# Performance work log

Hardware: AMD Instinct MI355X
Metric: run time of the kernel (lower is better)

Reference implementation:

```python
import jax, jax.numpy as jnp
import numpy as np
from math import lgamma

# ---- constants matching init_kwargs ----
HID_DIM = 512
LAT_DIM = 128
KAPPA = 50.0
NORM_EPS = 1.0
NORM_MAX = 2.0
BATCH = 65536

# ---- host-side constant KLD (scipy-free log Bessel via series) ----
def _log_iv(nu, k, M=300):
    m = np.arange(M)
    lg_fact = np.array([lgamma(i + 1.0) for i in m])
    lg_gam = np.array([lgamma(i + nu + 1.0) for i in m])
    logt = (2.0 * m + nu) * np.log(k / 2.0) - lg_fact - lg_gam
    mx = logt.max()
    return mx + np.log(np.exp(logt - mx).sum())

def _vmf_kld(k, d):
    # k*((iv(d/2+1,k)+iv(d/2,k)*d/(2k))/iv(d/2,k) - d/(2k)) + d*log(k)/2 - log(iv(d/2,k)) - loggamma(d/2+1) - d*log(2)/2
    ratio = np.exp(_log_iv(d / 2.0 + 1.0, k) - _log_iv(d / 2.0, k))
    return (k * (ratio + d / (2.0 * k) - d / (2.0 * k))
            + d * np.log(k) / 2.0 - _log_iv(d / 2.0, k)
            - lgamma(d / 2.0 + 1.0) - d * np.log(2.0) / 2.0)

def _uniform_kld(x1, x2, y1, y2):
    return np.log((y2 - y1) / (x2 - x1))

KLD_CONST = float(_vmf_kld(KAPPA, LAT_DIM) + _uniform_kld(0.0, NORM_EPS, 0.0, NORM_MAX))

# ---- batched vMF rejection sampling for the scalar weight w ----
def _sample_weight_batch(key, kappa, dim, shape):
    d = float(dim - 1)
    b = d / (np.sqrt(4.0 * kappa ** 2 + d * d) + 2.0 * kappa)
    x = (1.0 - b) / (1.0 + b)
    c = kappa * x + d * np.log(1.0 - x * x)

    def cond(st):
        return jnp.logical_not(jnp.all(st[2]))

    def body(st):
        key, w, acc = st
        key, kz, ku = jax.random.split(key, 3)
        z = jax.random.beta(kz, d / 2.0, d / 2.0, shape)
        wn = (1.0 - (1.0 + b) * z) / (1.0 - (1.0 - b) * z)
        u = jax.random.uniform(ku, shape)
        ok = (kappa * wn + d * jnp.log(1.0 - x * wn) - c) >= jnp.log(u)
        w = jnp.where(jnp.logical_and(jnp.logical_not(acc), ok), wn, w)
        return (key, w, jnp.logical_or(acc, ok))

    st0 = (key, jnp.zeros(shape, jnp.float32), jnp.zeros(shape, bool))
    _, w, _ = jax.lax.while_loop(cond, body, st0)
    return w


def setup_inputs() -> dict:
    key = jax.random.key(0)
    k1, k2 = jax.random.split(key)
    lat_code = jax.random.normal(k1, (BATCH, HID_DIM), dtype=jnp.float32)
    W_mu = jax.random.normal(k2, (LAT_DIM, HID_DIM), dtype=jnp.float32) * 0.02
    b_mu = jnp.zeros((LAT_DIM,), dtype=jnp.float32)
    return {"lat_code": lat_code, "W_mu": W_mu, "b_mu": b_mu, "n_sample": 4}


def reference(lat_code, W_mu, b_mu, n_sample):
    B = lat_code.shape[0]
    # estimate_param (norm_func=False branch)
    mu_lin = lat_code @ W_mu.T + b_mu                       # (B, L)
    norm = jnp.linalg.norm(mu_lin, axis=1, keepdims=True)   # (B, 1)
    redundant_norm = (1.0 - norm) ** 2                      # (B, 1)
    mu = mu_lin / norm                                      # unit directions

    # sample_cell, vectorized over (n_sample, B)
    kw, kv, kn = jax.random.split(jax.random.key(1), 3)
    w = _sample_weight_batch(kw, KAPPA, LAT_DIM, (n_sample, B))[..., None]  # (n,B,1)
    v = jax.random.normal(kv, (n_sample, B, LAT_DIM), dtype=jnp.float32)
    dot = jnp.sum(mu * v, axis=-1, keepdims=True)                           # (n,B,1)
    mu_n = jnp.linalg.norm(mu, axis=-1, keepdims=True)                      # ~1
    ortho = v - mu * (dot / mu_n)
    v_orth = ortho / jnp.linalg.norm(ortho, axis=-1, keepdims=True)
    noise = jax.random.uniform(kn, (n_sample, B, 1)) * NORM_EPS             # add_norm_noise
    norm_with_noise = 1.0 + noise                                           # norm=ones branch
    vecs = (v_orth * jnp.sqrt(1.0 - w * w) + mu * w) * norm_with_noise      # (n,B,L)

    kld = jnp.full((B,), KLD_CONST, dtype=lat_code.dtype)
    return (vecs, kld, mu, redundant_norm)
```

## Files before the change

kernel.cpp:

```cpp
#include <hip/hip_runtime.h>
#include <cmath>
#include <cstdint>


#define BTOT 65536
#define NSAMP 4
#define HID 512
#define LATD 128
#define NW 262144u

typedef _Float16 half8 __attribute__((ext_vector_type(8)));
typedef _Float16 half4 __attribute__((ext_vector_type(4)));
typedef float f32x4 __attribute__((ext_vector_type(4)));

__host__ __device__ __forceinline__ uint32_t rotl32(uint32_t v, int r){
  return (v << r) | (v >> (32 - r));
}

__host__ __device__ __forceinline__ void tf2(uint32_t k0, uint32_t k1,
                                             uint32_t x0, uint32_t x1,
                                             uint32_t& o0, uint32_t& o1){
  uint32_t ks2 = k0 ^ k1 ^ 0x1BD11BDAu;
  x0 += k0; x1 += k1;
  x0+=x1; x1=rotl32(x1,13); x1^=x0;
  x0+=x1; x1=rotl32(x1,15); x1^=x0;
  x0+=x1; x1=rotl32(x1,26); x1^=x0;
  x0+=x1; x1=rotl32(x1, 6); x1^=x0;
  x0+=k1; x1+=ks2+1u;
  x0+=x1; x1=rotl32(x1,17); x1^=x0;
  x0+=x1; x1=rotl32(x1,29); x1^=x0;
  x0+=x1; x1=rotl32(x1,16); x1^=x0;
  x0+=x1; x1=rotl32(x1,24); x1^=x0;
  x0+=ks2; x1+=k0+2u;
  x0+=x1; x1=rotl32(x1,13); x1^=x0;
  x0+=x1; x1=rotl32(x1,15); x1^=x0;
  x0+=x1; x1=rotl32(x1,26); x1^=x0;
  x0+=x1; x1=rotl32(x1, 6); x1^=x0;
  x0+=k0; x1+=k1+3u;
  x0+=x1; x1=rotl32(x1,17); x1^=x0;
  x0+=x1; x1=rotl32(x1,29); x1^=x0;
  x0+=x1; x1=rotl32(x1,16); x1^=x0;
  x0+=x1; x1=rotl32(x1,24); x1^=x0;
  x0+=k1; x1+=ks2+4u;
  x0+=x1; x1=rotl32(x1,13); x1^=x0;
  x0+=x1; x1=rotl32(x1,15); x1^=x0;
  x0+=x1; x1=rotl32(x1,26); x1^=x0;
  x0+=x1; x1=rotl32(x1, 6); x1^=x0;
  x0+=ks2; x1+=k0+5u;
  o0 = x0; o1 = x1;
}

__device__ __forceinline__ uint2 mkk(uint32_t a, uint32_t b){ uint2 r; r.x=a; r.y=b; return r; }

__device__ __forceinline__ uint2 p_split(uint2 k, uint32_t i){
  uint32_t o0,o1; tf2(k.x,k.y,0u,i,o0,o1); return mkk(o0,o1);
}
__device__ __forceinline__ uint32_t p_bits(uint2 k, uint32_t i){
  uint32_t o0,o1; tf2(k.x,k.y,0u,i,o0,o1); return o0^o1;
}

__device__ __forceinline__ float u01(uint32_t bits){
  return __uint_as_float((bits >> 9) | 0x3f800000u) - 1.0f;
}

__device__ __forceinline__ float erfinv_f(float x){
  float w = -log1pf(-x*x);
  float p;
  if (w < 5.0f){
    w -= 2.5f;
    p = 2.81022636e-08f;
    p = fmaf(p,w, 3.43273939e-07f);
    p = fmaf(p,w,-3.5233877e-06f);
    p = fmaf(p,w,-4.39150654e-06f);
    p = fmaf(p,w, 0.00021858087f);
    p = fmaf(p,w,-0.00125372503f);
    p = fmaf(p,w,-0.00417768164f);
    p = fmaf(p,w, 0.246640727f);
    p = fmaf(p,w, 1.50140941f);
  } else {
    w = sqrtf(w) - 3.0f;
    p = -0.000200214257f;
    p = fmaf(p,w, 0.000100950558f);
    p = fmaf(p,w, 0.00134934322f);
    p = fmaf(p,w,-0.00367342844f);
    p = fmaf(p,w, 0.00573950773f);
    p = fmaf(p,w,-0.0076224613f);
    p = fmaf(p,w, 0.00943887047f);
    p = fmaf(p,w, 1.00167406f);
    p = fmaf(p,w, 2.83297682f);
  }
  return p * x;
}

__device__ __forceinline__ float jnorm_from_bits(uint32_t bits){
  const float lo = -0.99999994f;
  float f = u01(bits);
  float un = fmaxf(lo, f*2.0f + lo);
  return 1.41421356f * erfinv_f(un);
}

__device__ __forceinline__ float jnorm_fast(uint32_t bits){
  const float lo = -0.99999994f;
  float f = u01(bits);
  float x = fmaxf(lo, f*2.0f + lo);
  float w = -0.69314718f * __builtin_amdgcn_logf(fmaf(-x, x, 1.0f));
  float p;
  if (w < 5.0f){
    w -= 2.5f;
    p = 2.81022636e-08f;
    p = fmaf(p,w, 3.43273939e-07f);
    p = fmaf(p,w,-3.5233877e-06f);
    p = fmaf(p,w,-4.39150654e-06f);
    p = fmaf(p,w, 0.00021858087f);
    p = fmaf(p,w,-0.00125372503f);
    p = fmaf(p,w,-0.00417768164f);
    p = fmaf(p,w, 0.246640727f);
    p = fmaf(p,w, 1.50140941f);
  } else {
    w = __builtin_amdgcn_sqrtf(w) - 3.0f;
    p = -0.000200214257f;
    p = fmaf(p,w, 0.000100950558f);
    p = fmaf(p,w, 0.00134934322f);
    p = fmaf(p,w,-0.00367342844f);
    p = fmaf(p,w, 0.00573950773f);
    p = fmaf(p,w,-0.0076224613f);
    p = fmaf(p,w, 0.00943887047f);
    p = fmaf(p,w, 1.00167406f);
    p = fmaf(p,w, 2.83297682f);
  }
  return 1.41421356f * (p * x);
}

__device__ float loggamma_a635(uint2 ek){
  const float dg = 63.5f - (1.0f/3.0f);
  const float cg = (1.0f/3.0f) / sqrtf(dg);
  uint2 key = p_split(ek, 0);
  float lg = 0.0f;
  for (int it=0; it<64; ++it){
    uint2 xk = p_split(key, 1);
    uint2 uk = p_split(key, 2);
    uint2 sub2 = p_split(xk, 1);
    float x = 1.41421356f * erfinv_f(fmaxf(-0.99999994f,
                u01(p_bits(sub2, 0))*2.0f + (-0.99999994f)));
    float v = 1.0f + x*cg;
    float X = x*x;
    float V = v*v*v;
    float U = u01(p_bits(uk, 0));
    bool rej = (U >= 1.0f - 0.0331f*(X*X)) &&
               (logf(U) >= 0.5f*X + dg*((1.0f - V) + logf(V)));
    if (!rej){ lg = logf(dg) + logf(V); break; }
    key = p_split(key, 0);
  }
  return lg;
}

__global__ __launch_bounds__(256) void bprep_kernel(const float* __restrict__ W,
                                                    unsigned short* __restrict__ Bhi,
                                                    unsigned short* __restrict__ Blo){
  int t = blockIdx.x*256 + threadIdx.x;
  int l = t >> 7, k4 = t & 127;
  int k0 = k4*4;
  float4 wv = *(const float4*)(W + (size_t)l*HID + k0);
  half4 h, lo;
  float b0 = (float)(_Float16)wv.x; h.x = (_Float16)wv.x; lo.x = (_Float16)((wv.x-b0)*2048.0f);
  float b1 = (float)(_Float16)wv.y; h.y = (_Float16)wv.y; lo.y = (_Float16)((wv.y-b1)*2048.0f);
  float b2 = (float)(_Float16)wv.z; h.z = (_Float16)wv.z; lo.z = (_Float16)((wv.z-b2)*2048.0f);
  float b3 = (float)(_Float16)wv.w; h.w = (_Float16)wv.w; lo.w = (_Float16)((wv.w-b3)*2048.0f);
  int c = k0 >> 5, g = (k0 & 31) >> 3, j0 = k0 & 7;
  int nf = l >> 4, n15 = l & 15;
  size_t idx = ((size_t)((c*8 + nf)*4 + g)*16 + n15)*8 + j0;
  *(half4*)(Bhi + idx) = h;
  *(half4*)(Blo + idx) = lo;
}

__global__ __launch_bounds__(256) void mu_kernel(const float* __restrict__ lat,
                                                 const unsigned short* __restrict__ Bhi_g,
                                                 const unsigned short* __restrict__ Blo_g,
                                                 const float* __restrict__ bmu,
                                                 float* __restrict__ muo,
                                                 float* __restrict__ kldo,
                                                 float* __restrict__ rno,
                                                 float kldv){
  __shared__ __align__(16) char smem[26624];
  _Float16* Ahi = (_Float16*)smem;
  _Float16* Alo = (_Float16*)(smem + 5120);
  _Float16* Blh = (_Float16*)(smem + 10240);
  _Float16* Bll = (_Float16*)(smem + 18432);

  const int tid = threadIdx.x;
  const int w   = tid >> 6;
  const int lane = tid & 63;
  const int q = lane >> 4, n15 = lane & 15;
  const int b0 = blockIdx.x * 64;
  const float4* latg = (const float4*)lat;

  f32x4 acc1a[4][2], acc1b[4][2], acc2[4][2];
  #pragma unroll
  for (int rf=0;rf<4;++rf)
    #pragma unroll
    for (int nl=0;nl<2;++nl){
      acc1a[rf][nl] = (f32x4)0.0f;
      acc1b[rf][nl] = (f32x4)0.0f;
      acc2[rf][nl]  = (f32x4)0.0f;
    }

  for (int c=0;c<16;++c){
    __syncthreads();
    #pragma unroll
    for (int p=0;p<2;++p){
      int flat = p*256 + tid;
      int row = flat >> 3, k4 = flat & 7;
      float4 lv = latg[(size_t)(b0+row)*(HID/4) + c*8 + k4];
      half4 h, lo;
      float r0=(float)(_Float16)lv.x; h.x=(_Float16)lv.x; lo.x=(_Float16)((lv.x-r0)*2048.0f);
      float r1=(float)(_Float16)lv.y; h.y=(_Float16)lv.y; lo.y=(_Float16)((lv.y-r1)*2048.0f);
      float r2=(float)(_Float16)lv.z; h.z=(_Float16)lv.z; lo.z=(_Float16)((lv.z-r2)*2048.0f);
      float r3=(float)(_Float16)lv.w; h.w=(_Float16)lv.w; lo.w=(_Float16)((lv.w-r3)*2048.0f);
      *(half4*)(Ahi + row*40 + k4*4) = h;
      *(half4*)(Alo + row*40 + k4*4) = lo;
    }
    {
      const short4* sh = (const short4*)Bhi_g + (size_t)c*1024;
      const short4* sl = (const short4*)Blo_g + (size_t)c*1024;
      short4* dh = (short4*)Blh;
      short4* dl = (short4*)Bll;
      #pragma unroll
      for (int p=0;p<4;++p){
        dh[tid + p*256] = sh[tid + p*256];
        dl[tid + p*256] = sl[tid + p*256];
      }
    }
    __syncthreads();

    half8 bh[2], bl[2];
    #pragma unroll
    for (int nl=0;nl<2;++nl){
      int nf = w*2 + nl;
      bh[nl] = *(const half8*)(Blh + ((nf*4 + q)*16 + n15)*8);
      bl[nl] = *(const half8*)(Bll + ((nf*4 + q)*16 + n15)*8);
    }
    #pragma unroll
    for (int rf=0;rf<4;++rf){
      half8 ah = *(const half8*)(Ahi + (rf*16 + n15)*40 + q*8);
      half8 al = *(const half8*)(Alo + (rf*16 + n15)*40 + q*8);
      #pragma unroll
      for (int nl=0;nl<2;++nl){
        if (c < 8)
          acc1a[rf][nl] = __builtin_amdgcn_mfma_f32_16x16x32_f16(ah, bh[nl], acc1a[rf][nl], 0,0,0);
        else
          acc1b[rf][nl] = __builtin_amdgcn_mfma_f32_16x16x32_f16(ah, bh[nl], acc1b[rf][nl], 0,0,0);
        acc2[rf][nl] = __builtin_amdgcn_mfma_f32_16x16x32_f16(ah, bl[nl], acc2[rf][nl], 0,0,0);
        acc2[rf][nl] = __builtin_amdgcn_mfma_f32_16x16x32_f16(al, bh[nl], acc2[rf][nl], 0,0,0);
      }
    }
  }

  __syncthreads();
  double* nbuf  = (double*)smem;
  double* normd = (double*)(smem + 2048);

  double bias[2];
  #pragma unroll
  for (int nl=0;nl<2;++nl) bias[nl] = (double)bmu[w*32 + nl*16 + n15];

  double val[4][2][4];
  double part[4][4];
  #pragma unroll
  for (int rf=0;rf<4;++rf){
    #pragma unroll
    for (int r=0;r<4;++r){
      double s = 0.0;
      #pragma unroll
      for (int nl=0;nl<2;++nl){
        double v = (double)acc1a[rf][nl][r] + (double)acc1b[rf][nl][r]
                 + (double)acc2[rf][nl][r]*(1.0/2048.0) + bias[nl];
        val[rf][nl][r] = v;
        s += v*v;
      }
      part[rf][r] = s;
    }
  }
  #pragma unroll
  for (int rf=0;rf<4;++rf)
    #pragma unroll
    for (int r=0;r<4;++r){
      double t = part[rf][r];
      t += __shfl_xor(t, 1, 64);
      t += __shfl_xor(t, 2, 64);
      t += __shfl_xor(t, 4, 64);
      t += __shfl_xor(t, 8, 64);
      part[rf][r] = t;
    }
  if (n15 == 0){
    #pragma unroll
    for (int rf=0;rf<4;++rf)
      #pragma unroll
      for (int r=0;r<4;++r)
        nbuf[w*64 + rf*16 + q*4 + r] = part[rf][r];
  }
  __syncthreads();
  if (tid < 64){
    double tot = nbuf[tid] + nbuf[64+tid] + nbuf[128+tid] + nbuf[192+tid];
    double nd = sqrt(tot);
    normd[tid] = nd;
    double om = 1.0 - nd;
    rno[b0 + tid]  = (float)(om*om);
    kldo[b0 + tid] = kldv;
  }
  __syncthreads();
  #pragma unroll
  for (int rf=0;rf<4;++rf){
    #pragma unroll
    for (int r=0;r<4;++r){
      double nd = normd[rf*16 + q*4 + r];
      int m = b0 + rf*16 + q*4 + r;
      #pragma unroll
      for (int nl=0;nl<2;++nl)
        muo[(size_t)m*LATD + w*32 + nl*16 + n15] = (float)(val[rf][nl][r]/nd);
    }
  }
}

__global__ __launch_bounds__(256) void wood_kernel(float* __restrict__ wbuf,
                                                   float* __restrict__ nwnbuf,
                                                   uint2 kw, uint2 kn,
                                                   float onepb, float onemb,
                                                   float xf, float cf){
  uint32_t j = blockIdx.x*256u + threadIdx.x;
  nwnbuf[j] = 1.0f + u01(p_bits(kn, j));
  uint2 key = kw;
  float w = 0.0f;
  for (int it=0; it<64; ++it){
    uint2 kz = p_split(key, 1);
    uint2 ku = p_split(key, 2);
    uint2 ka = p_split(kz, 0);
    uint2 kb = p_split(kz, 1);
    float lga = loggamma_a635(p_split(ka, j));
    float lgb = loggamma_a635(p_split(kb, j));
    float mx  = fmaxf(lga, lgb);
    float lab = mx + log1pf(expf(-fabsf(lga-lgb)));
    float z   = expf(lga - lab);
    float wn  = (1.0f - onepb*z) / (1.0f - onemb*z);
    float u   = u01(p_bits(ku, j));
    bool ok = (50.0f*wn + 127.0f*logf(1.0f - xf*wn) - cf) >= logf(u);
    if (ok){ w = wn; break; }
    key = p_split(key, 0);
  }
  wbuf[j] = w;
}

#define SWZ8(mask) { _Pragma("unroll")                                        \
  for (int i=0;i<8;++i)                                                       \
    red[i] += __int_as_float(__builtin_amdgcn_ds_swizzle(                     \
                 __float_as_int(red[i]), mask)); }

__global__ __launch_bounds__(256) void vec_kernel(const float* __restrict__ mu,
                                                  const float* __restrict__ wbuf,
                                                  const float* __restrict__ nwnbuf,
                                                  float* __restrict__ vecs,
                                                  uint2 kv){
  uint32_t gid  = blockIdx.x*256u + threadIdx.x;
  uint32_t b    = gid >> 6;
  uint32_t lane = gid & 63u;
  float2 m = ((const float2*)mu)[(size_t)b*64 + lane];
  float wv[4], nv[4];
  #pragma unroll
  for (int s=0;s<4;s++){ wv[s]=wbuf[(uint32_t)s*BTOT+b]; nv[s]=nwnbuf[(uint32_t)s*BTOT+b]; }

  float v[4][2];
  #pragma unroll
  for (int s=0;s<4;++s){
    uint32_t jj = ((uint32_t)s*BTOT + b)*128u + lane*2u;
    v[s][0] = jnorm_fast(p_bits(kv, jj));
    v[s][1] = jnorm_fast(p_bits(kv, jj+1u));
  }

  float red[8];
  #pragma unroll
  for (int s=0;s<4;s++){
    red[s]   = fmaf(m.x, v[s][0], m.y*v[s][1]);
    red[4+s] = fmaf(v[s][0], v[s][0], v[s][1]*v[s][1]);
  }
  SWZ8(0x041F)
  SWZ8(0x081F)
  SWZ8(0x101F)
  SWZ8(0x201F)
  SWZ8(0x401F)
  #pragma unroll
  for (int i=0;i<8;++i) red[i] += __shfl_xor(red[i], 32, 64);

  #pragma unroll
  for (int s=0;s<4;s++){
    float dot = red[s];
    float on2 = fmaf(-dot, dot, red[4+s]);
    float a   = __builtin_amdgcn_rsqf(on2)
              * __builtin_amdgcn_sqrtf(fmaf(-wv[s], wv[s], 1.0f));
    float mw  = wv[s];
    float f0 = fmaf(fmaf(-m.x, dot, v[s][0]), a, m.x*mw) * nv[s];
    float f1 = fmaf(fmaf(-m.y, dot, v[s][1]), a, m.y*mw) * nv[s];
    ((float2*)vecs)[((size_t)s*BTOT + b)*64 + lane] = make_float2(f0,f1);
  }
}

static double log_iv_host(double nu, double k){
  double logt[300];
  double mx = -1e300;
  for (int m=0;m<300;m++){
    double md = (double)m;
    double t = (2.0*md + nu)*std::log(k/2.0) - std::lgamma(md+1.0) - std::lgamma(md+nu+1.0);
    logt[m]=t; if (t>mx) mx=t;
  }
  double s=0.0;
  for (int m=0;m<300;m++) s += std::exp(logt[m]-mx);
  return mx + std::log(s);
}

extern "C" void kernel_launch(void* const* d_in, const int* in_sizes, int n_in,
                              void* d_out, int out_size, void* d_ws, size_t ws_size,
                              hipStream_t stream) {
  const float* lat = (const float*)d_in[0];
  const float* W   = (const float*)d_in[1];
  const float* bmu = (const float*)d_in[2];
  float* out  = (float*)d_out;
  float* vecs = out;
  float* kld  = out + (size_t)NSAMP*BTOT*LATD;
  float* mu   = kld + BTOT;
  float* rn   = mu + (size_t)BTOT*LATD;

  float* wbuf   = (float*)d_ws;
  float* nwnbuf = wbuf + NW;
  unsigned short* Bhi = (unsigned short*)(nwnbuf + NW);
  unsigned short* Blo = Bhi + HID*LATD;

  uint32_t o0,o1;
  uint2 kw, kv, kn;
  tf2(0u,1u,0u,0u,o0,o1); kw.x=o0; kw.y=o1;
  tf2(0u,1u,0u,1u,o0,o1); kv.x=o0; kv.y=o1;
  tf2(0u,1u,0u,2u,o0,o1); kn.x=o0; kn.y=o1;

  const double dd=127.0, kp=50.0;
  double bb = dd/(std::sqrt(4.0*kp*kp+dd*dd)+2.0*kp);
  double xx = (1.0-bb)/(1.0+bb);
  double cc = kp*xx + dd*std::log(1.0-xx*xx);
  float onepb=(float)(1.0+bb), onemb=(float)(1.0-bb), xf=(float)xx, cf=(float)cc;

  double li64 = log_iv_host(64.0, 50.0);
  double li65 = log_iv_host(65.0, 50.0);
  double ratio = std::exp(li65 - li64);
  const double dK = 128.0;
  double kld_d = kp*((ratio + dK/(2.0*kp)) - dK/(2.0*kp))
               + dK*std::log(kp)/2.0 - li64
               - std::lgamma(dK/2.0+1.0) - dK*std::log(2.0)/2.0
               + std::log((2.0-0.0)/(1.0-0.0));
  float kldv = (float)kld_d;

  bprep_kernel<<<(HID*LATD/4)/256, 256, 0, stream>>>(W, Bhi, Blo);
  wood_kernel<<<NW/256, 256, 0, stream>>>(wbuf, nwnbuf, kw, kn, onepb, onemb, xf, cf);
  mu_kernel<<<BTOT/64, 256, 0, stream>>>(lat, Bhi, Blo, bmu, mu, kld, rn, kldv);
  vec_kernel<<<(BTOT*64)/256, 256, 0, stream>>>(mu, wbuf, nwnbuf, vecs, kv);
}
```

Before: 186.5 us.

## Fuse rejection sampler into mu GEMM kernel and use DPP for row reductions

Merges the wood rejection-sampling kernel into the mu projection kernel. Odd blocks run the sampler and even blocks run the GEMM, so the ALU-heavy sampling can overlap the matrix work and one launch plus its tail are removed. The rotate-left helper now uses the alignbit builtin on device. In vec_kernel, four of the five ds_swizzle reduction steps become DPP quad_perm and mirror adds. The trade-off is that sampler blocks also reserve the GEMM's shared memory, which may lower occupancy for those blocks.

```diff
diff --git a/kernel.cpp b/kernel.cpp
--- a/kernel.cpp
+++ b/kernel.cpp
@@ -14,7 +14,11 @@
 typedef float f32x4 __attribute__((ext_vector_type(4)));
 
 __host__ __device__ __forceinline__ uint32_t rotl32(uint32_t v, int r){
+#if defined(__HIP_DEVICE_COMPILE__)
+  return __builtin_amdgcn_alignbit(v, v, 32 - r);
+#else
   return (v << r) | (v >> (32 - r));
+#endif
 }
 
 __host__ __device__ __forceinline__ void tf2(uint32_t k0, uint32_t k1,
@@ -92,13 +96,6 @@
   return p * x;
 }
 
-__device__ __forceinline__ float jnorm_from_bits(uint32_t bits){
-  const float lo = -0.99999994f;
-  float f = u01(bits);
-  float un = fmaxf(lo, f*2.0f + lo);
-  return 1.41421356f * erfinv_f(un);
-}
-
 __device__ __forceinline__ float jnorm_fast(uint32_t bits){
   const float lo = -0.99999994f;
   float f = u01(bits);
@@ -173,25 +170,56 @@
   *(half4*)(Blo + idx) = lo;
 }
 
-__global__ __launch_bounds__(256) void mu_kernel(const float* __restrict__ lat,
-                                                 const unsigned short* __restrict__ Bhi_g,
-                                                 const unsigned short* __restrict__ Blo_g,
-                                                 const float* __restrict__ bmu,
-                                                 float* __restrict__ muo,
-                                                 float* __restrict__ kldo,
-                                                 float* __restrict__ rno,
-                                                 float kldv){
+__global__ __launch_bounds__(256) void muwood_kernel(const float* __restrict__ lat,
+                                                     const unsigned short* __restrict__ Bhi_g,
+                                                     const unsigned short* __restrict__ Blo_g,
+                                                     const float* __restrict__ bmu,
+                                                     float* __restrict__ muo,
+                                                     float* __restrict__ kldo,
+                                                     float* __restrict__ rno,
+                                                     float kldv,
+                                                     float* __restrict__ wbuf,
+                                                     float* __restrict__ nwnbuf,
+                                                     uint2 kw, uint2 kn,
+                                                     float onepb, float onemb,
+                                                     float xf, float cf){
   __shared__ __align__(16) char smem[26624];
+  const int tid = threadIdx.x;
+
+  if (blockIdx.x & 1){
+    uint32_t j = (blockIdx.x >> 1)*256u + tid;
+    nwnbuf[j] = 1.0f + u01(p_bits(kn, j));
+    uint2 key = kw;
+    float w = 0.0f;
+    for (int it=0; it<64; ++it){
+      uint2 kz = p_split(key, 1);
+      uint2 ku = p_split(key, 2);
+      uint2 ka = p_split(kz, 0);
+      uint2 kb = p_split(kz, 1);
+      float lga = loggamma_a635(p_split(ka, j));
+      float lgb = loggamma_a635(p_split(kb, j));
+      float mx  = fmaxf(lga, lgb);
+      float lab = mx + log1pf(expf(-fabsf(lga-lgb)));
+      float z   = expf(lga - lab);
+      float wn  = (1.0f - onepb*z) / (1.0f - onemb*z);
+      float u   = u01(p_bits(ku, j));
+      bool ok = (50.0f*wn + 127.0f*logf(1.0f - xf*wn) - cf) >= logf(u);
+      if (ok){ w = wn; break; }
+      key = p_split(key, 0);
+    }
+    wbuf[j] = w;
+    return;
+  }
+
   _Float16* Ahi = (_Float16*)smem;
   _Float16* Alo = (_Float16*)(smem + 5120);
   _Float16* Blh = (_Float16*)(smem + 10240);
   _Float16* Bll = (_Float16*)(smem + 18432);
 
-  const int tid = threadIdx.x;
   const int w   = tid >> 6;
   const int lane = tid & 63;
   const int q = lane >> 4, n15 = lane & 15;
-  const int b0 = blockIdx.x * 64;
+  const int b0 = (blockIdx.x >> 1) * 64;
   const float4* latg = (const float4*)lat;
 
   f32x4 acc1a[4][2], acc1b[4][2], acc2[4][2];
@@ -321,38 +349,11 @@
   }
 }
 
-__global__ __launch_bounds__(256) void wood_kernel(float* __restrict__ wbuf,
-                                                   float* __restrict__ nwnbuf,
-                                                   uint2 kw, uint2 kn,
-                                                   float onepb, float onemb,
-                                                   float xf, float cf){
-  uint32_t j = blockIdx.x*256u + threadIdx.x;
-  nwnbuf[j] = 1.0f + u01(p_bits(kn, j));
-  uint2 key = kw;
-  float w = 0.0f;
-  for (int it=0; it<64; ++it){
-    uint2 kz = p_split(key, 1);
-    uint2 ku = p_split(key, 2);
-    uint2 ka = p_split(kz, 0);
-    uint2 kb = p_split(kz, 1);
-    float lga = loggamma_a635(p_split(ka, j));
-    float lgb = loggamma_a635(p_split(kb, j));
-    float mx  = fmaxf(lga, lgb);
-    float lab = mx + log1pf(expf(-fabsf(lga-lgb)));
-    float z   = expf(lga - lab);
-    float wn  = (1.0f - onepb*z) / (1.0f - onemb*z);
-    float u   = u01(p_bits(ku, j));
-    bool ok = (50.0f*wn + 127.0f*logf(1.0f - xf*wn) - cf) >= logf(u);
-    if (ok){ w = wn; break; }
-    key = p_split(key, 0);
-  }
-  wbuf[j] = w;
-}
-
-#define SWZ8(mask) { _Pragma("unroll")                                        \
-  for (int i=0;i<8;++i)                                                       \
-    red[i] += __int_as_float(__builtin_amdgcn_ds_swizzle(                     \
-                 __float_as_int(red[i]), mask)); }
+template<int CTRL>
+__device__ __forceinline__ float dpp_add(float x){
+  int v = __builtin_amdgcn_update_dpp(0, __float_as_int(x), CTRL, 0xF, 0xF, true);
+  return x + __int_as_float(v);
+}
 
 __global__ __launch_bounds__(256) void vec_kernel(const float* __restrict__ mu,
                                                   const float* __restrict__ wbuf,
@@ -381,11 +382,18 @@
     red[s]   = fmaf(m.x, v[s][0], m.y*v[s][1]);
     red[4+s] = fmaf(v[s][0], v[s][0], v[s][1]*v[s][1]);
   }
-  SWZ8(0x041F)
-  SWZ8(0x081F)
-  SWZ8(0x101F)
-  SWZ8(0x201F)
-  SWZ8(0x401F)
+  #pragma unroll
+  for (int i=0;i<8;++i) red[i] = dpp_add<0xB1>(red[i]);
+  #pragma unroll
+  for (int i=0;i<8;++i) red[i] = dpp_add<0x4E>(red[i]);
+  #pragma unroll
+  for (int i=0;i<8;++i) red[i] = dpp_add<0x141>(red[i]);
+  #pragma unroll
+  for (int i=0;i<8;++i) red[i] = dpp_add<0x140>(red[i]);
+  #pragma unroll
+  for (int i=0;i<8;++i)
+    red[i] += __int_as_float(__builtin_amdgcn_ds_swizzle(
+                 __float_as_int(red[i]), 0x401F));
   #pragma unroll
   for (int i=0;i<8;++i) red[i] += __shfl_xor(red[i], 32, 64);
 
@@ -455,7 +463,7 @@
   float kldv = (float)kld_d;
 
   bprep_kernel<<<(HID*LATD/4)/256, 256, 0, stream>>>(W, Bhi, Blo);
-  wood_kernel<<<NW/256, 256, 0, stream>>>(wbuf, nwnbuf, kw, kn, onepb, onemb, xf, cf);
-  mu_kernel<<<BTOT/64, 256, 0, stream>>>(lat, Bhi, Blo, bmu, mu, kld, rn, kldv);
+  muwood_kernel<<<2048, 256, 0, stream>>>(lat, Bhi, Blo, bmu, mu, kld, rn, kldv,
+                                          wbuf, nwnbuf, kw, kn, onepb, onemb, xf, cf);
   vec_kernel<<<(BTOT*64)/256, 256, 0, stream>>>(mu, wbuf, nwnbuf, vecs, kv);
 }
```

Measured after the change: 192.4 us. 3.2% more time.
